# Kernel tuning notes

Measured on AMD Instinct MI355X. Metric: run time of the kernel, lower is better.

## Reference

```python
import jax, jax.numpy as jnp
import numpy as np

N, C, H, O, NUM_CLASSES = 4096, 768, 512, 50, 1


def setup_inputs() -> dict:
    key = jax.random.key(0)
    ks = jax.random.split(key, 8)
    x = jax.random.normal(ks[0], (N, C), dtype=jnp.float32)
    labels = jax.random.randint(ks[1], (N,), 0, 2, dtype=jnp.int64)
    W1 = jax.random.normal(ks[2], (C, H), dtype=jnp.float32) / np.sqrt(C)
    b1 = jnp.zeros((H,), dtype=jnp.float32)
    W2 = jax.random.normal(ks[3], (H, O), dtype=jnp.float32) / np.sqrt(H)
    b2 = jnp.zeros((O,), dtype=jnp.float32)
    fcW = jax.random.normal(ks[4], (C + O, NUM_CLASSES), dtype=jnp.float32) / np.sqrt(C + O)
    fcb = jnp.zeros((NUM_CLASSES,), dtype=jnp.float32)
    return {"x": x, "labels": labels, "W1": W1, "b1": b1, "W2": W2, "b2": b2, "fcW": fcW, "fcb": fcb}


def _build_graph(x, labels):
    # similarity-threshold edge construction (dense masked form of the python double loop)
    sim = x @ x.T                                   # [N, N]
    n = x.shape[0]
    diff = labels[:, None] != labels[None, :]       # cross-label pairs
    cnt = jnp.sum(diff)
    s = jnp.sum(jnp.where(diff, sim, 0.0))
    threshold = jnp.where(cnt > 0, s / cnt.astype(sim.dtype), jnp.asarray(0.0, sim.dtype))
    eye = jnp.eye(n, dtype=bool)
    same = (labels[:, None] == labels[None, :]) & ~eye
    edge_mask = same & (sim <= threshold)           # symmetric (sim symmetric)
    loss_mask = edge_mask & (jnp.arange(n)[:, None] < jnp.arange(n)[None, :])  # i<j pairs
    adj = jax.lax.stop_gradient(edge_mask.astype(x.dtype))
    # GCN normalization with self-loops
    a = adj + jnp.eye(n, dtype=x.dtype)
    dinv = jax.lax.rsqrt(jnp.sum(a, axis=1))        # deg >= 1
    norm_adj = dinv[:, None] * a * dinv[None, :]
    return norm_adj, loss_mask


def reference(x, labels, W1, b1, W2, b2, fcW, fcb):
    norm_adj, loss_mask = _build_graph(x, labels)
    h = jax.nn.relu(norm_adj @ (x @ W1) + b1)       # conv1 + relu
    g = norm_adj @ (h @ W2) + b2                    # conv2
    f_g = jnp.concatenate([x, g], axis=-1)          # [N, C+O]
    out = f_g @ fcW + fcb                           # [N, 1]
    return out, f_g, loss_mask, x
```

## Files before the change

kernel.cpp:

```cpp
#include <hip/hip_runtime.h>
#include <hip/hip_bf16.h>
#include <math.h>

#define NN 4096
#define CD 768
#define HD 512
#define OD 50
#define FGD 818

typedef short short8 __attribute__((ext_vector_type(8)));
typedef float f32x4 __attribute__((ext_vector_type(4)));
typedef unsigned short us4 __attribute__((ext_vector_type(4)));
typedef unsigned short ushortT;
typedef unsigned char uchar;
typedef unsigned long long u64;

__device__ inline ushortT f2bf(float v) {
    __hip_bfloat16 b = __float2bfloat16(v);
    return *(ushortT*)&b;
}
__device__ inline float bf2f(ushortT u) {
    __hip_bfloat16 b = *(__hip_bfloat16*)&u;
    return __bfloat162float(b);
}
__device__ inline float dinv_of(int d) {
    return (float)(1.0 / sqrt((double)(1 + d)));
}

__global__ __launch_bounds__(256) void gsum_kernel(const float* __restrict__ x,
                                                   const int* __restrict__ labels,
                                                   double* __restrict__ gsum) {
    int b = blockIdx.x;
    int t = threadIdx.x;
    double a0[3] = {0, 0, 0}, a1[3] = {0, 0, 0};
    for (int rr = 0; rr < 16; ++rr) {
        int row = b * 16 + rr;
        int lab = labels[row];
#pragma unroll
        for (int s = 0; s < 3; ++s) {
            double v = (double)x[(size_t)row * CD + t + s * 256];
            if (lab == 0) a0[s] += v; else a1[s] += v;
        }
    }
#pragma unroll
    for (int s = 0; s < 3; ++s) {
        atomicAdd(&gsum[t + s * 256], a0[s]);
        atomicAdd(&gsum[768 + t + s * 256], a1[s]);
    }
}

__global__ __launch_bounds__(256) void gdot_kernel(const double* __restrict__ gsum,
                                                   const int* __restrict__ labels,
                                                   double* __restrict__ scal) {
    int t = threadIdx.x;
    double d = 0.0;
    for (int c = t; c < CD; c += 256) d += gsum[c] * gsum[768 + c];
    int n0 = 0;
    for (int i = t; i < NN; i += 256) n0 += (labels[i] == 0) ? 1 : 0;
    for (int off = 32; off; off >>= 1) {
        d += __shfl_down(d, off);
        n0 += __shfl_down(n0, off);
    }
    __shared__ double sd[4];
    __shared__ int sn[4];
    int wid = t >> 6, lane = t & 63;
    if (lane == 0) { sd[wid] = d; sn[wid] = n0; }
    __syncthreads();
    if (t == 0) {
        double D = sd[0] + sd[1] + sd[2] + sd[3];
        double N0 = (double)(sn[0] + sn[1] + sn[2] + sn[3]);
        scal[0] = 2.0 * D;
        scal[1] = 2.0 * N0 * ((double)NN - N0);
    }
}

#define BAND 4e-3
#define RC_CAP (1 << 18)

__global__ __launch_bounds__(256) void sim_fused(
    const ushortT* __restrict__ xh, const ushortT* __restrict__ xl,
    const int* __restrict__ labels, const double* __restrict__ scal,
    u64* __restrict__ abbits, float* __restrict__ lm, int* __restrict__ deg,
    int* __restrict__ rc_cnt, int* __restrict__ rc_list) {
    int bid = blockIdx.x;
    int sid = (bid & 7) * 260 + (bid >> 3);
    int sby = 0, rem = sid;
    for (; sby < 8; ++sby) {
        int rowsz = 36 + (7 - sby) * 64;
        if (rem < rowsz) break;
        rem -= rowsz;
    }
    int sbx, iby, ibx;
    if (rem < 36) {
        sbx = sby;
        iby = 0;
        while (rem >= 8 - iby) { rem -= 8 - iby; ++iby; }
        ibx = iby + rem;
    } else {
        rem -= 36;
        sbx = sby + 1 + (rem >> 6);
        int u = rem & 63;
        iby = u >> 3; ibx = u & 7;
    }
    int by = sby * 8 + iby, bx = sbx * 8 + ibx;
    bool diag = (bx == by);

    __shared__ ushortT lds[4 * 64 * 72];
    __shared__ int larr[128];
    int tid = threadIdx.x;
    int lane = tid & 63;
    int w = tid >> 6;
    int wr = w >> 1, wc = w & 1;
    int m = lane & 15, quad = lane >> 4;
    int row0 = by * 64, col0 = bx * 64;

    if (tid < 64) larr[tid] = labels[row0 + tid];
    else if (tid < 128) larr[tid] = labels[col0 + tid - 64];

    f32x4 acc[2][2] = {{{0.f, 0.f, 0.f, 0.f}, {0.f, 0.f, 0.f, 0.f}},
                       {{0.f, 0.f, 0.f, 0.f}, {0.f, 0.f, 0.f, 0.f}}};

    const size_t rowbase = (size_t)row0 * CD;
    const size_t colbase = (size_t)col0 * CD;
    short8 rg[2][4];
#pragma unroll
    for (int tt = 0; tt < 2; ++tt) {
        int id2 = tid + tt * 256;
        int row = id2 >> 3, c8 = (id2 & 7) * 8;
        rg[tt][0] = *(const short8*)&xh[rowbase + (size_t)row * CD + c8];
        rg[tt][1] = *(const short8*)&xl[rowbase + (size_t)row * CD + c8];
        rg[tt][2] = *(const short8*)&xh[colbase + (size_t)row * CD + c8];
        rg[tt][3] = *(const short8*)&xl[colbase + (size_t)row * CD + c8];
    }

    for (int k0 = 0; k0 < CD; k0 += 64) {
        __syncthreads();
#pragma unroll
        for (int tt = 0; tt < 2; ++tt) {
            int id2 = tid + tt * 256;
            int row = id2 >> 3, c8 = (id2 & 7) * 8;
            *(short8*)&lds[0 * 4608 + row * 72 + c8] = rg[tt][0];
            *(short8*)&lds[1 * 4608 + row * 72 + c8] = rg[tt][1];
            *(short8*)&lds[2 * 4608 + row * 72 + c8] = rg[tt][2];
            *(short8*)&lds[3 * 4608 + row * 72 + c8] = rg[tt][3];
        }
        __syncthreads();
        if (k0 + 64 < CD) {
#pragma unroll
            for (int tt = 0; tt < 2; ++tt) {
                int id2 = tid + tt * 256;
                int row = id2 >> 3, c8 = (id2 & 7) * 8 + k0 + 64;
                rg[tt][0] = *(const short8*)&xh[rowbase + (size_t)row * CD + c8];
                rg[tt][1] = *(const short8*)&xl[rowbase + (size_t)row * CD + c8];
                rg[tt][2] = *(const short8*)&xh[colbase + (size_t)row * CD + c8];
                rg[tt][3] = *(const short8*)&xl[colbase + (size_t)row * CD + c8];
            }
        }
#pragma unroll
        for (int ks = 0; ks < 2; ++ks) {
            short8 ah[2], al[2], bh[2], bl[2];
#pragma unroll
            for (int i = 0; i < 2; ++i) {
                int ro = (wr * 32 + i * 16 + m) * 72 + ks * 32 + quad * 8;
                ah[i] = *(const short8*)&lds[0 * 4608 + ro];
                al[i] = *(const short8*)&lds[1 * 4608 + ro];
            }
#pragma unroll
            for (int j = 0; j < 2; ++j) {
                int co = (wc * 32 + j * 16 + m) * 72 + ks * 32 + quad * 8;
                bh[j] = *(const short8*)&lds[2 * 4608 + co];
                bl[j] = *(const short8*)&lds[3 * 4608 + co];
            }
#pragma unroll
            for (int i = 0; i < 2; ++i)
#pragma unroll
                for (int j = 0; j < 2; ++j) {
                    acc[i][j] = __builtin_amdgcn_mfma_f32_16x16x32_bf16(
                        ah[i], bh[j], acc[i][j], 0, 0, 0);
                    acc[i][j] = __builtin_amdgcn_mfma_f32_16x16x32_bf16(
                        ah[i], bl[j], acc[i][j], 0, 0, 0);
                    acc[i][j] = __builtin_amdgcn_mfma_f32_16x16x32_bf16(
                        al[i], bh[j], acc[i][j], 0, 0, 0);
                }
        }
    }
    __syncthreads();

    double thrd;
    {
        double cnt = scal[1];
        thrd = (cnt > 0.0) ? (scal[0] / cnt) : 0.0;
    }
    uchar* flags = (uchar*)lds;
#pragma unroll
    for (int i = 0; i < 2; ++i)
#pragma unroll
        for (int j = 0; j < 2; ++j) {
#pragma unroll
            for (int r = 0; r < 4; ++r) {
                int row = wr * 32 + i * 16 + quad * 4 + r;
                int col = wc * 32 + j * 16 + m;
                bool same = (larr[row] == larr[64 + col]);
                bool selfp = ((row0 + row) == (col0 + col));
                bool edge = false;
                if (same && !selfp) {
                    double s = (double)acc[i][j][r];
                    if (s <= thrd - BAND) {
                        edge = true;
                    } else if (s <= thrd + BAND) {
                        edge = (s <= thrd);
                        int enc = ((row0 + row) << 12) | (col0 + col) |
                                  (diag ? 0 : (1 << 24)) |
                                  (edge ? (1 << 25) : 0);
                        int idx = atomicAdd(rc_cnt, 1);
                        if (idx < RC_CAP) rc_list[idx] = enc;
                    }
                }
                flags[row * 68 + col] = edge ? 1 : 0;
            }
        }
    __syncthreads();

    {
        int r = tid >> 2, q = tid & 3;
        int cnti = 0;
        unsigned int bits16 = 0;
#pragma unroll
        for (int s = 0; s < 4; ++s) {
            int cb = q * 16 + s * 4;
            float4 f;
#pragma unroll
            for (int k2 = 0; k2 < 4; ++k2) {
                int c = cb + k2;
                bool fl = flags[r * 68 + c] != 0;
                cnti += fl ? 1 : 0;
                if (fl || (diag && r == c)) bits16 |= 1u << (s * 4 + k2);
                ((float*)&f)[k2] = (fl && (row0 + r < col0 + c)) ? 1.0f : 0.0f;
            }
            *(float4*)&lm[(size_t)(row0 + r) * NN + col0 + cb] = f;
        }
        unsigned int s1 = __shfl_down(bits16, 1);
        unsigned int s2 = __shfl_down(bits16, 2);
        unsigned int s3 = __shfl_down(bits16, 3);
        cnti += __shfl_down(cnti, 1);
        cnti += __shfl_down(cnti, 2);
        if (q == 0) {
            u64 u = (u64)bits16 | ((u64)s1 << 16) | ((u64)s2 << 32) |
                    ((u64)s3 << 48);
            abbits[(size_t)(row0 + r) * 64 + bx] = u;
            if (cnti) atomicAdd(&deg[row0 + r], cnti);
        }
    }

    if (!diag) {
        int c = tid >> 2, q = tid & 3;
        int cnti = 0;
        unsigned int bits16 = 0;
        float4 fz = {0.0f, 0.0f, 0.0f, 0.0f};
#pragma unroll
        for (int s = 0; s < 4; ++s) {
            int rb = q * 16 + s * 4;
#pragma unroll
            for (int k2 = 0; k2 < 4; ++k2) {
                bool fl = flags[(rb + k2) * 68 + c] != 0;
                cnti += fl ? 1 : 0;
                if (fl) bits16 |= 1u << (s * 4 + k2);
            }
            *(float4*)&lm[(size_t)(col0 + c) * NN + row0 + rb] = fz;
        }
        unsigned int s1 = __shfl_down(bits16, 1);
        unsigned int s2 = __shfl_down(bits16, 2);
        unsigned int s3 = __shfl_down(bits16, 3);
        cnti += __shfl_down(cnti, 1);
        cnti += __shfl_down(cnti, 2);
        if (q == 0) {
            u64 u = (u64)bits16 | ((u64)s1 << 16) | ((u64)s2 << 32) |
                    ((u64)s3 << 48);
            abbits[(size_t)(col0 + c) * 64 + by] = u;
            if (cnti) atomicAdd(&deg[col0 + c], cnti);
        }
    }
}

__global__ __launch_bounds__(256) void rc_fix(
    const float* __restrict__ x, const double* __restrict__ scal,
    const int* __restrict__ rc_cnt, const int* __restrict__ rc_list,
    u64* __restrict__ abbits, float* __restrict__ lm, int* __restrict__ deg) {
    int cnt = *rc_cnt;
    if (cnt > RC_CAP) cnt = RC_CAP;
    double thrd;
    {
        double c = scal[1];
        thrd = (c > 0.0) ? (scal[0] / c) : 0.0;
    }
    int lane = threadIdx.x & 63;
    int wid = (blockIdx.x * 256 + threadIdx.x) >> 6;
    int nw = (gridDim.x * 256) >> 6;
    for (int e = wid; e < cnt; e += nw) {
        int enc = rc_list[e];
        int c = enc & 0xFFF;
        int r = (enc >> 12) & 0xFFF;
        bool mirror = (enc >> 24) & 1;
        bool prov = (enc >> 25) & 1;
        const float* xi = x + (size_t)r * CD;
        const float* xj = x + (size_t)c * CD;
        double d = 0.0;
#pragma unroll
        for (int s = 0; s < 12; ++s)
            d += (double)xi[lane + s * 64] * (double)xj[lane + s * 64];
        for (int off = 32; off; off >>= 1) d += __shfl_down(d, off);
        if (lane == 0) {
            bool exact = (d <= thrd);
            if (exact != prov) {
                u64 mk = 1ull << (c & 63);
                if (exact) atomicOr(&abbits[(size_t)r * 64 + (c >> 6)], mk);
                else       atomicAnd(&abbits[(size_t)r * 64 + (c >> 6)], ~mk);
                lm[(size_t)r * NN + c] = (exact && r < c) ? 1.0f : 0.0f;
                int dlt = exact ? 1 : -1;
                atomicAdd(&deg[r], dlt);
                if (mirror) {
                    u64 mk2 = 1ull << (r & 63);
                    if (exact) atomicOr(&abbits[(size_t)c * 64 + (r >> 6)], mk2);
                    else       atomicAnd(&abbits[(size_t)c * 64 + (r >> 6)], ~mk2);
                    atomicAdd(&deg[c], dlt);
                }
            }
        }
    }
}

__global__ __launch_bounds__(256) void prep_kernel(
    const float* __restrict__ x, const float* __restrict__ W1,
    const float* __restrict__ W2, float* __restrict__ fg, float* __restrict__ xo,
    ushortT* __restrict__ xh, ushortT* __restrict__ xl, ushortT* __restrict__ w1t,
    ushortT* __restrict__ w2t) {
    int b = blockIdx.x;
    if (b < 4096) {
        int t = threadIdx.x;
        if (t < 192) {
            float4 v = *(const float4*)&x[(size_t)b * CD + t * 4];
            *(float4*)&xo[(size_t)b * CD + t * 4] = v;
            fg[(size_t)b * FGD + t * 4 + 0] = v.x;
            fg[(size_t)b * FGD + t * 4 + 1] = v.y;
            fg[(size_t)b * FGD + t * 4 + 2] = v.z;
            fg[(size_t)b * FGD + t * 4 + 3] = v.w;
            us4 hh, ll;
            float* vp = (float*)&v;
#pragma unroll
            for (int k = 0; k < 4; ++k) {
                ushortT h = f2bf(vp[k]);
                ((ushortT*)&hh)[k] = h;
                ((ushortT*)&ll)[k] = f2bf(vp[k] - bf2f(h));
            }
            *(us4*)&xh[(size_t)b * CD + t * 4] = hh;
            *(us4*)&xl[(size_t)b * CD + t * 4] = ll;
        }
        return;
    }
    __shared__ float tT[32][33];
    const float* P;
    ushortT* T;
    int K, N, Npad, k0, n0;
    if (b < 4480) {
        int bb = b - 4096;
        P = W1; T = w1t; K = CD; N = HD; Npad = HD;
        k0 = (bb % 24) * 32; n0 = (bb / 24) * 32;
    } else {
        int bb = b - 4480;
        P = W2; T = w2t; K = HD; N = OD; Npad = 64;
        k0 = (bb % 16) * 32; n0 = (bb / 16) * 32;
    }
    int tx = threadIdx.x & 31, ty = threadIdx.x >> 5;
#pragma unroll
    for (int s = 0; s < 4; ++s) {
        int k = k0 + ty + s * 8, n = n0 + tx;
        tT[ty + s * 8][tx] = (k < K && n < N) ? P[(size_t)k * N + n] : 0.0f;
    }
    __syncthreads();
#pragma unroll
    for (int s = 0; s < 4; ++s) {
        int n = n0 + ty + s * 8, k = k0 + tx;
        if (n < Npad && k < K) T[(size_t)n * K + k] = f2bf(tT[tx][ty + s * 8]);
    }
}

template <bool RELU, bool HASBIAS, int EPI>
__global__ __launch_bounds__(256) void gemm_bf16(
    const ushortT* __restrict__ A, const ushortT* __restrict__ B,
    ushortT* __restrict__ Cb, int M, int Nn, int K, int ldc,
    const int* __restrict__ deg, const float* __restrict__ bias) {
    __shared__ ushortT lds[2 * 64 * 72];
    int tid = threadIdx.x;
    int lane = tid & 63;
    int w = tid >> 6;
    int wr = w >> 1, wc = w & 1;
    int m = lane & 15, quad = lane >> 4;
    int row0 = blockIdx.y * 64, col0 = blockIdx.x * 64;

    f32x4 acc[2][2] = {{{0.f, 0.f, 0.f, 0.f}, {0.f, 0.f, 0.f, 0.f}},
                       {{0.f, 0.f, 0.f, 0.f}, {0.f, 0.f, 0.f, 0.f}}};

    for (int k0 = 0; k0 < K; k0 += 64) {
#pragma unroll
        for (int t = 0; t < 2; ++t) {
            int id2 = tid + t * 256;
            int row = id2 >> 3, c8 = (id2 & 7) * 8;
            *(short8*)&lds[row * 72 + c8] =
                *(const short8*)&A[(size_t)(row0 + row) * K + k0 + c8];
            *(short8*)&lds[4608 + row * 72 + c8] =
                *(const short8*)&B[(size_t)(col0 + row) * K + k0 + c8];
        }
        __syncthreads();
#pragma unroll
        for (int ks = 0; ks < 2; ++ks) {
            short8 af[2], bf[2];
#pragma unroll
            for (int i = 0; i < 2; ++i)
                af[i] = *(const short8*)&lds[(wr * 32 + i * 16 + m) * 72 +
                                             ks * 32 + quad * 8];
#pragma unroll
            for (int j = 0; j < 2; ++j)
                bf[j] = *(const short8*)&lds[4608 + (wc * 32 + j * 16 + m) * 72 +
                                             ks * 32 + quad * 8];
#pragma unroll
            for (int i = 0; i < 2; ++i)
#pragma unroll
                for (int j = 0; j < 2; ++j)
                    acc[i][j] = __builtin_amdgcn_mfma_f32_16x16x32_bf16(
                        af[i], bf[j], acc[i][j], 0, 0, 0);
        }
        __syncthreads();
    }

    if (EPI == 2) {
        ushortT* Th = lds;
#pragma unroll
        for (int i = 0; i < 2; ++i)
#pragma unroll
            for (int j = 0; j < 2; ++j)
#pragma unroll
                for (int r = 0; r < 4; ++r) {
                    int row = wr * 32 + i * 16 + quad * 4 + r;
                    int col = wc * 32 + j * 16 + m;
                    float dv = dinv_of(deg[row0 + row]);
                    Th[col * 72 + row] = f2bf(acc[i][j][r] * dv);
                }
        __syncthreads();
#pragma unroll
        for (int t = 0; t < 2; ++t) {
            int id2 = tid + t * 256;
            int cc = id2 >> 3, chunk = id2 & 7;
            *(short8*)&Cb[(size_t)(col0 + cc) * M + row0 + chunk * 8] =
                *(const short8*)&Th[cc * 72 + chunk * 8];
        }
    } else {
#pragma unroll
        for (int i = 0; i < 2; ++i)
#pragma unroll
            for (int j = 0; j < 2; ++j)
#pragma unroll
                for (int r = 0; r < 4; ++r) {
                    int row = wr * 32 + i * 16 + quad * 4 + r;
                    int col = wc * 32 + j * 16 + m;
                    int gr = row0 + row, gc = col0 + col;
                    if (gc < Nn) {
                        float v = acc[i][j][r] * dinv_of(deg[gr]);
                        if (HASBIAS) v += bias[gc];
                        if (RELU) v = fmaxf(v, 0.0f);
                        Cb[(size_t)gr * ldc + gc] = f2bf(v);
                    }
                }
    }
}

__global__ __launch_bounds__(256) void gemm_part(
    const ushortT* __restrict__ A, const ushortT* __restrict__ B,
    float* __restrict__ P, int M, int K, int KC) {
    __shared__ ushortT lds[2 * 64 * 72];
    int tid = threadIdx.x;
    int lane = tid & 63;
    int w = tid >> 6;
    int wr = w >> 1, wc = w & 1;
    int m = lane & 15, quad = lane >> 4;
    int kb = blockIdx.x;
    int row0 = blockIdx.y * 64;
    int kbase = kb * KC;

    f32x4 acc[2][2] = {{{0.f, 0.f, 0.f, 0.f}, {0.f, 0.f, 0.f, 0.f}},
                       {{0.f, 0.f, 0.f, 0.f}, {0.f, 0.f, 0.f, 0.f}}};

    for (int k0 = 0; k0 < KC; k0 += 64) {
#pragma unroll
        for (int t = 0; t < 2; ++t) {
            int id2 = tid + t * 256;
            int row = id2 >> 3, c8 = (id2 & 7) * 8;
            *(short8*)&lds[row * 72 + c8] =
                *(const short8*)&A[(size_t)(row0 + row) * K + kbase + k0 + c8];
            *(short8*)&lds[4608 + row * 72 + c8] =
                *(const short8*)&B[(size_t)row * K + kbase + k0 + c8];
        }
        __syncthreads();
#pragma unroll
        for (int ks = 0; ks < 2; ++ks) {
            short8 af[2], bf[2];
#pragma unroll
            for (int i = 0; i < 2; ++i)
                af[i] = *(const short8*)&lds[(wr * 32 + i * 16 + m) * 72 +
                                             ks * 32 + quad * 8];
#pragma unroll
            for (int j = 0; j < 2; ++j)
                bf[j] = *(const short8*)&lds[4608 + (wc * 32 + j * 16 + m) * 72 +
                                             ks * 32 + quad * 8];
#pragma unroll
            for (int i = 0; i < 2; ++i)
#pragma unroll
                for (int j = 0; j < 2; ++j)
                    acc[i][j] = __builtin_amdgcn_mfma_f32_16x16x32_bf16(
                        af[i], bf[j], acc[i][j], 0, 0, 0);
        }
        __syncthreads();
    }
#pragma unroll
    for (int i = 0; i < 2; ++i)
#pragma unroll
        for (int j = 0; j < 2; ++j)
#pragma unroll
            for (int r = 0; r < 4; ++r) {
                int row = wr * 32 + i * 16 + quad * 4 + r;
                int col = wc * 32 + j * 16 + m;
                P[((size_t)kb * M + row0 + row) * 64 + col] = acc[i][j][r];
            }
}

__global__ __launch_bounds__(256) void gemm_partB(
    const u64* __restrict__ Abits, const ushortT* __restrict__ B,
    float* __restrict__ P, int M, int K, int KC) {
    __shared__ ushortT lds[2 * 64 * 72];
    int tid = threadIdx.x;
    int lane = tid & 63;
    int w = tid >> 6;
    int wr = w >> 1, wc = w & 1;
    int m = lane & 15, quad = lane >> 4;
    int kb = blockIdx.x;
    int row0 = blockIdx.y * 64;
    int kbase = kb * KC;
    int er = tid >> 2, eq = tid & 3;

    f32x4 acc[2][2] = {{{0.f, 0.f, 0.f, 0.f}, {0.f, 0.f, 0.f, 0.f}},
                       {{0.f, 0.f, 0.f, 0.f}, {0.f, 0.f, 0.f, 0.f}}};

    for (int k0 = 0; k0 < KC; k0 += 64) {
#pragma unroll
        for (int t = 0; t < 2; ++t) {
            int id2 = tid + t * 256;
            int row = id2 >> 3, c8 = (id2 & 7) * 8;
            *(short8*)&lds[4608 + row * 72 + c8] =
                *(const short8*)&B[(size_t)row * K + kbase + k0 + c8];
        }
        {
            u64 bits = Abits[(size_t)(row0 + er) * 64 + ((kbase + k0) >> 6)];
            unsigned int half = (unsigned int)(bits >> (eq * 16)) & 0xFFFFu;
            short8 v0, v1;
#pragma unroll
            for (int k = 0; k < 8; ++k) {
                ((ushortT*)&v0)[k] =
                    ((half >> k) & 1) ? (ushortT)0x3F80 : (ushortT)0;
                ((ushortT*)&v1)[k] =
                    ((half >> (k + 8)) & 1) ? (ushortT)0x3F80 : (ushortT)0;
            }
            *(short8*)&lds[er * 72 + eq * 16] = v0;
            *(short8*)&lds[er * 72 + eq * 16 + 8] = v1;
        }
        __syncthreads();
#pragma unroll
        for (int ks = 0; ks < 2; ++ks) {
            short8 af[2], bf[2];
#pragma unroll
            for (int i = 0; i < 2; ++i)
                af[i] = *(const short8*)&lds[(wr * 32 + i * 16 + m) * 72 +
                                             ks * 32 + quad * 8];
#pragma unroll
            for (int j = 0; j < 2; ++j)
                bf[j] = *(const short8*)&lds[4608 + (wc * 32 + j * 16 + m) * 72 +
                                             ks * 32 + quad * 8];
#pragma unroll
            for (int i = 0; i < 2; ++i)
#pragma unroll
                for (int j = 0; j < 2; ++j)
                    acc[i][j] = __builtin_amdgcn_mfma_f32_16x16x32_bf16(
                        af[i], bf[j], acc[i][j], 0, 0, 0);
        }
        __syncthreads();
    }
#pragma unroll
    for (int i = 0; i < 2; ++i)
#pragma unroll
        for (int j = 0; j < 2; ++j)
#pragma unroll
            for (int r = 0; r < 4; ++r) {
                int row = wr * 32 + i * 16 + quad * 4 + r;
                int col = wc * 32 + j * 16 + m;
                P[((size_t)kb * M + row0 + row) * 64 + col] = acc[i][j][r];
            }
}

__global__ __launch_bounds__(256) void gemm_partWB(
    const u64* __restrict__ Abits, const ushortT* __restrict__ B,
    float* __restrict__ P, int M, int K, int KC, int ldP) {
    __shared__ ushortT lds[2 * 64 * 72];
    int tid = threadIdx.x;
    int lane = tid & 63;
    int w = tid >> 6;
    int wr = w >> 1, wc = w & 1;
    int m = lane & 15, quad = lane >> 4;
    int col0 = blockIdx.x * 64;
    int row0 = blockIdx.y * 64;
    int kb = blockIdx.z;
    int kbase = kb * KC;
    int er = tid >> 2, eq = tid & 3;

    f32x4 acc[2][2] = {{{0.f, 0.f, 0.f, 0.f}, {0.f, 0.f, 0.f, 0.f}},
                       {{0.f, 0.f, 0.f, 0.f}, {0.f, 0.f, 0.f, 0.f}}};

    for (int k0 = 0; k0 < KC; k0 += 64) {
#pragma unroll
        for (int t = 0; t < 2; ++t) {
            int id2 = tid + t * 256;
            int row = id2 >> 3, c8 = (id2 & 7) * 8;
            *(short8*)&lds[4608 + row * 72 + c8] =
                *(const short8*)&B[(size_t)(col0 + row) * K + kbase + k0 + c8];
        }
        {
            u64 bits = Abits[(size_t)(row0 + er) * 64 + ((kbase + k0) >> 6)];
            unsigned int half = (unsigned int)(bits >> (eq * 16)) & 0xFFFFu;
            short8 v0, v1;
#pragma unroll
            for (int k = 0; k < 8; ++k) {
                ((ushortT*)&v0)[k] =
                    ((half >> k) & 1) ? (ushortT)0x3F80 : (ushortT)0;
                ((ushortT*)&v1)[k] =
                    ((half >> (k + 8)) & 1) ? (ushortT)0x3F80 : (ushortT)0;
            }
            *(short8*)&lds[er * 72 + eq * 16] = v0;
            *(short8*)&lds[er * 72 + eq * 16 + 8] = v1;
        }
        __syncthreads();
#pragma unroll
        for (int ks = 0; ks < 2; ++ks) {
            short8 af[2], bf[2];
#pragma unroll
            for (int i = 0; i < 2; ++i)
                af[i] = *(const short8*)&lds[(wr * 32 + i * 16 + m) * 72 +
                                             ks * 32 + quad * 8];
#pragma unroll
            for (int j = 0; j < 2; ++j)
                bf[j] = *(const short8*)&lds[4608 + (wc * 32 + j * 16 + m) * 72 +
                                             ks * 32 + quad * 8];
#pragma unroll
            for (int i = 0; i < 2; ++i)
#pragma unroll
                for (int j = 0; j < 2; ++j)
                    acc[i][j] = __builtin_amdgcn_mfma_f32_16x16x32_bf16(
                        af[i], bf[j], acc[i][j], 0, 0, 0);
        }
        __syncthreads();
    }
#pragma unroll
    for (int i = 0; i < 2; ++i)
#pragma unroll
        for (int j = 0; j < 2; ++j)
#pragma unroll
            for (int r = 0; r < 4; ++r) {
                int row = wr * 32 + i * 16 + quad * 4 + r;
                int col = wc * 32 + j * 16 + m;
                P[((size_t)kb * M + row0 + row) * ldP + col0 + col] =
                    acc[i][j][r];
            }
}

__global__ __launch_bounds__(256) void k5_epi(const float* __restrict__ P5,
                                              const int* __restrict__ deg,
                                              const float* __restrict__ b1,
                                              ushortT* __restrict__ hb) {
    int tid = threadIdx.x;
    int cg = tid & 127;
    int rr = tid >> 7;
#pragma unroll
    for (int p = 0; p < 2; ++p) {
        int r = blockIdx.x * 4 + p * 2 + rr;
        float dv = dinv_of(deg[r]);
        float4 s = {0.f, 0.f, 0.f, 0.f};
#pragma unroll
        for (int kb = 0; kb < 4; ++kb) {
            float4 v = *(const float4*)&P5[((size_t)kb * NN + r) * HD + cg * 4];
            s.x += v.x; s.y += v.y; s.z += v.z; s.w += v.w;
        }
        float4 bv = *(const float4*)&b1[cg * 4];
        us4 o;
        o[0] = f2bf(fmaxf(s.x * dv + bv.x, 0.f));
        o[1] = f2bf(fmaxf(s.y * dv + bv.y, 0.f));
        o[2] = f2bf(fmaxf(s.z * dv + bv.z, 0.f));
        o[3] = f2bf(fmaxf(s.w * dv + bv.w, 0.f));
        *(us4*)&hb[(size_t)r * HD + cg * 4] = o;
    }
}

__global__ __launch_bounds__(256) void k6_epi(const float* __restrict__ P6,
                                              const int* __restrict__ deg,
                                              ushortT* __restrict__ hw2sT) {
    __shared__ ushortT Th[64 * 72];
    int row0 = blockIdx.x * 64;
    int tid = threadIdx.x;
    int rl = tid >> 2, q = tid & 3;
    float dv = dinv_of(deg[row0 + rl]);
#pragma unroll
    for (int s = 0; s < 16; ++s) {
        int c = q * 16 + s;
        float v = 0.f;
#pragma unroll
        for (int kb = 0; kb < 4; ++kb)
            v += P6[((size_t)kb * NN + row0 + rl) * 64 + c];
        Th[c * 72 + rl] = f2bf(v * dv);
    }
    __syncthreads();
#pragma unroll
    for (int t = 0; t < 2; ++t) {
        int id2 = tid + t * 256;
        int cc = id2 >> 3, chunk = id2 & 7;
        *(short8*)&hw2sT[(size_t)cc * NN + row0 + chunk * 8] =
            *(const short8*)&Th[cc * 72 + chunk * 8];
    }
}

__global__ __launch_bounds__(256) void k7_epi_out(
    const float* __restrict__ P7, const int* __restrict__ deg,
    const float* __restrict__ b2, const float* __restrict__ fcW,
    const float* __restrict__ fcb, float* __restrict__ fg,
    float* __restrict__ out) {
    int row0 = blockIdx.x * 64;
    int tid = threadIdx.x;
    int rl = tid >> 2, q = tid & 3;
    int r = row0 + rl;
    float dv = dinv_of(deg[r]);
    float sg = 0.f;
#pragma unroll
    for (int s = 0; s < 16; ++s) {
        int c = q * 16 + s;
        if (c < OD) {
            float v = 0.f;
#pragma unroll
            for (int kb = 0; kb < 8; ++kb)
                v += P7[((size_t)kb * NN + r) * 64 + c];
            v = v * dv + b2[c];
            fg[(size_t)r * FGD + CD + c] = v;
            sg += v * fcW[CD + c];
        }
    }
    const float* fr = fg + (size_t)r * FGD;
    float sx = 0.f;
    for (int k = q * 192; k < (q + 1) * 192; k += 2) {
        float2 vv = *(const float2*)&fr[k];
        float2 ww = *(const float2*)&fcW[k];
        sx += vv.x * ww.x + vv.y * ww.y;
    }
    float s = sx + sg;
    s += __shfl_down(s, 1);
    s += __shfl_down(s, 2);
    if (q == 0) out[r] = s + fcb[0];
}

extern "C" void kernel_launch(void* const* d_in, const int* in_sizes, int n_in,
                              void* d_out, int out_size, void* d_ws, size_t ws_size,
                              hipStream_t stream) {
    const float* x = (const float*)d_in[0];
    const int* labels = (const int*)d_in[1];
    const float* W1 = (const float*)d_in[2];
    const float* b1 = (const float*)d_in[3];
    const float* W2 = (const float*)d_in[4];
    const float* b2 = (const float*)d_in[5];
    const float* fcW = (const float*)d_in[6];
    const float* fcb = (const float*)d_in[7];
    float* outp = (float*)d_out;

    const size_t o_out = 0;
    const size_t o_fg = 4096;
    const size_t o_lm = o_fg + (size_t)NN * FGD;
    const size_t o_x = o_lm + (size_t)NN * NN;

    char* ws = (char*)d_ws;
    size_t off = 0;
    u64* abbits = (u64*)(ws + off); off += (size_t)NN * 64 * 8;
    ushortT* xh = (ushortT*)(ws + off); off += (size_t)NN * CD * 2;
    ushortT* xl = (ushortT*)(ws + off); off += (size_t)NN * CD * 2;
    ushortT* w1t = (ushortT*)(ws + off); off += (size_t)HD * CD * 2;
    ushortT* xw1sT = (ushortT*)(ws + off); off += (size_t)HD * NN * 2;
    ushortT* hb = (ushortT*)(ws + off); off += (size_t)NN * HD * 2;
    ushortT* w2t = (ushortT*)(ws + off); off += (size_t)64 * HD * 2;
    ushortT* hw2sT = (ushortT*)(ws + off); off += (size_t)64 * NN * 2;
    char* zbase = ws + off;
    int* deg = (int*)(ws + off); off += (size_t)NN * 4;
    double* gsum = (double*)(ws + off); off += 1536 * 8;
    double* scal = (double*)(ws + off); off += 16;
    int* rc_cnt = (int*)(ws + off); off += 16;
    size_t zbytes = (size_t)NN * 4 + 1536 * 8 + 16 + 16;
    char* uni = ws + off;
    int* rc_list = (int*)uni;
    float* P5 = (float*)uni;
    float* P6 = (float*)uni;
    float* P7 = (float*)uni;
    off += (size_t)4 * NN * HD * 4;

    hipMemsetAsync(zbase, 0, zbytes, stream);

    prep_kernel<<<4512, 256, 0, stream>>>(x, W1, W2, outp + o_fg, outp + o_x, xh, xl,
                                          w1t, w2t);

    gsum_kernel<<<256, 256, 0, stream>>>(x, labels, gsum);
    gdot_kernel<<<1, 256, 0, stream>>>(gsum, labels, scal);

    sim_fused<<<2080, 256, 0, stream>>>(xh, xl, labels, scal, abbits, outp + o_lm,
                                        deg, rc_cnt, rc_list);

    rc_fix<<<512, 256, 0, stream>>>(x, scal, rc_cnt, rc_list, abbits, outp + o_lm,
                                    deg);

    gemm_bf16<false, false, 2><<<dim3(HD / 64, NN / 64), 256, 0, stream>>>(
        xh, w1t, xw1sT, NN, HD, CD, 0, deg, nullptr);

    gemm_partWB<<<dim3(HD / 64, NN / 64, 4), 256, 0, stream>>>(
        abbits, xw1sT, P5, NN, NN, NN / 4, HD);
    k5_epi<<<NN / 4, 256, 0, stream>>>(P5, deg, b1, hb);

    gemm_part<<<dim3(4, NN / 64), 256, 0, stream>>>(hb, w2t, P6, NN, HD, HD / 4);
    k6_epi<<<NN / 64, 256, 0, stream>>>(P6, deg, hw2sT);

    gemm_partB<<<dim3(8, NN / 64), 256, 0, stream>>>(abbits, hw2sT, P7, NN, NN,
                                                     NN / 8);
    k7_epi_out<<<NN / 64, 256, 0, stream>>>(P7, deg, b2, fcW, fcb, outp + o_fg,
                                            outp + o_out);
}
```

Baseline: 322.2 us.

## Use single fp16 MFMA for similarity GEMM and widen split-K partitions

Replaces the three-pass bf16 hi/lo split product in the similarity kernel with one fp16 MFMA pass on an fp16 copy of x. This cuts MFMA work, LDS footprint and global loads by roughly half or more. The recheck band widens from 4e-3 to 0.10 so the rc_fix pass can correct borderline threshold decisions, which may push far more pairs into that exact-recheck path. Separately, split-K factors for the conv2 GEMMs double (4→8 and 8→16 partitions) to add parallelism, with the epilogues summing more partials.

Result: slower. 424.8 us (+31.8%).

```diff
diff --git a/kernel.cpp b/kernel.cpp
--- a/kernel.cpp
+++ b/kernel.cpp
@@ -9,6 +9,7 @@
 #define FGD 818
 
 typedef short short8 __attribute__((ext_vector_type(8)));
+typedef _Float16 half8 __attribute__((ext_vector_type(8)));
 typedef float f32x4 __attribute__((ext_vector_type(4)));
 typedef unsigned short us4 __attribute__((ext_vector_type(4)));
 typedef unsigned short ushortT;
@@ -74,13 +75,13 @@
     }
 }
 
-#define BAND 4e-3
+#define BAND 0.10
 #define RC_CAP (1 << 18)
 
 __global__ __launch_bounds__(256) void sim_fused(
-    const ushortT* __restrict__ xh, const ushortT* __restrict__ xl,
-    const int* __restrict__ labels, const double* __restrict__ scal,
-    u64* __restrict__ abbits, float* __restrict__ lm, int* __restrict__ deg,
+    const ushortT* __restrict__ xf, const int* __restrict__ labels,
+    const double* __restrict__ scal, u64* __restrict__ abbits,
+    float* __restrict__ lm, int* __restrict__ deg,
     int* __restrict__ rc_cnt, int* __restrict__ rc_list) {
     int bid = blockIdx.x;
     int sid = (bid & 7) * 260 + (bid >> 3);
@@ -105,7 +106,7 @@
     int by = sby * 8 + iby, bx = sbx * 8 + ibx;
     bool diag = (bx == by);
 
-    __shared__ ushortT lds[4 * 64 * 72];
+    __shared__ ushortT lds[2 * 64 * 72];
     __shared__ int larr[128];
     int tid = threadIdx.x;
     int lane = tid & 63;
@@ -122,15 +123,13 @@
 
     const size_t rowbase = (size_t)row0 * CD;
     const size_t colbase = (size_t)col0 * CD;
-    short8 rg[2][4];
+    short8 rg[2][2];
 #pragma unroll
     for (int tt = 0; tt < 2; ++tt) {
         int id2 = tid + tt * 256;
         int row = id2 >> 3, c8 = (id2 & 7) * 8;
-        rg[tt][0] = *(const short8*)&xh[rowbase + (size_t)row * CD + c8];
-        rg[tt][1] = *(const short8*)&xl[rowbase + (size_t)row * CD + c8];
-        rg[tt][2] = *(const short8*)&xh[colbase + (size_t)row * CD + c8];
-        rg[tt][3] = *(const short8*)&xl[colbase + (size_t)row * CD + c8];
+        rg[tt][0] = *(const short8*)&xf[rowbase + (size_t)row * CD + c8];
+        rg[tt][1] = *(const short8*)&xf[colbase + (size_t)row * CD + c8];
     }
 
     for (int k0 = 0; k0 < CD; k0 += 64) {
@@ -141,8 +140,6 @@
             int row = id2 >> 3, c8 = (id2 & 7) * 8;
             *(short8*)&lds[0 * 4608 + row * 72 + c8] = rg[tt][0];
             *(short8*)&lds[1 * 4608 + row * 72 + c8] = rg[tt][1];
-            *(short8*)&lds[2 * 4608 + row * 72 + c8] = rg[tt][2];
-            *(short8*)&lds[3 * 4608 + row * 72 + c8] = rg[tt][3];
         }
         __syncthreads();
         if (k0 + 64 < CD) {
@@ -150,38 +147,27 @@
             for (int tt = 0; tt < 2; ++tt) {
                 int id2 = tid + tt * 256;
                 int row = id2 >> 3, c8 = (id2 & 7) * 8 + k0 + 64;
-                rg[tt][0] = *(const short8*)&xh[rowbase + (size_t)row * CD + c8];
-                rg[tt][1] = *(const short8*)&xl[rowbase + (size_t)row * CD + c8];
-                rg[tt][2] = *(const short8*)&xh[colbase + (size_t)row * CD + c8];
-                rg[tt][3] = *(const short8*)&xl[colbase + (size_t)row * CD + c8];
+                rg[tt][0] = *(const short8*)&xf[rowbase + (size_t)row * CD + c8];
+                rg[tt][1] = *(const short8*)&xf[colbase + (size_t)row * CD + c8];
             }
         }
 #pragma unroll
         for (int ks = 0; ks < 2; ++ks) {
-            short8 ah[2], al[2], bh[2], bl[2];
-#pragma unroll
-            for (int i = 0; i < 2; ++i) {
-                int ro = (wr * 32 + i * 16 + m) * 72 + ks * 32 + quad * 8;
-                ah[i] = *(const short8*)&lds[0 * 4608 + ro];
-                al[i] = *(const short8*)&lds[1 * 4608 + ro];
-            }
-#pragma unroll
-            for (int j = 0; j < 2; ++j) {
-                int co = (wc * 32 + j * 16 + m) * 72 + ks * 32 + quad * 8;
-                bh[j] = *(const short8*)&lds[2 * 4608 + co];
-                bl[j] = *(const short8*)&lds[3 * 4608 + co];
-            }
-#pragma unroll
-            for (int i = 0; i < 2; ++i)
-#pragma unroll
-                for (int j = 0; j < 2; ++j) {
-                    acc[i][j] = __builtin_amdgcn_mfma_f32_16x16x32_bf16(
+            half8 ah[2], bh[2];
+#pragma unroll
+            for (int i = 0; i < 2; ++i)
+                ah[i] = *(const half8*)&lds[(wr * 32 + i * 16 + m) * 72 +
+                                            ks * 32 + quad * 8];
+#pragma unroll
+            for (int j = 0; j < 2; ++j)
+                bh[j] = *(const half8*)&lds[4608 + (wc * 32 + j * 16 + m) * 72 +
+                                            ks * 32 + quad * 8];
+#pragma unroll
+            for (int i = 0; i < 2; ++i)
+#pragma unroll
+                for (int j = 0; j < 2; ++j)
+                    acc[i][j] = __builtin_amdgcn_mfma_f32_16x16x32_f16(
                         ah[i], bh[j], acc[i][j], 0, 0, 0);
-                    acc[i][j] = __builtin_amdgcn_mfma_f32_16x16x32_bf16(
-                        ah[i], bl[j], acc[i][j], 0, 0, 0);
-                    acc[i][j] = __builtin_amdgcn_mfma_f32_16x16x32_bf16(
-                        al[i], bh[j], acc[i][j], 0, 0, 0);
-                }
         }
     }
     __syncthreads();
@@ -332,7 +318,7 @@
 __global__ __launch_bounds__(256) void prep_kernel(
     const float* __restrict__ x, const float* __restrict__ W1,
     const float* __restrict__ W2, float* __restrict__ fg, float* __restrict__ xo,
-    ushortT* __restrict__ xh, ushortT* __restrict__ xl, ushortT* __restrict__ w1t,
+    ushortT* __restrict__ xh, ushortT* __restrict__ xf, ushortT* __restrict__ w1t,
     ushortT* __restrict__ w2t) {
     int b = blockIdx.x;
     if (b < 4096) {
@@ -344,16 +330,16 @@
             fg[(size_t)b * FGD + t * 4 + 1] = v.y;
             fg[(size_t)b * FGD + t * 4 + 2] = v.z;
             fg[(size_t)b * FGD + t * 4 + 3] = v.w;
-            us4 hh, ll;
+            us4 hh, ff;
             float* vp = (float*)&v;
 #pragma unroll
             for (int k = 0; k < 4; ++k) {
-                ushortT h = f2bf(vp[k]);
-                ((ushortT*)&hh)[k] = h;
-                ((ushortT*)&ll)[k] = f2bf(vp[k] - bf2f(h));
+                ((ushortT*)&hh)[k] = f2bf(vp[k]);
+                _Float16 g = (_Float16)vp[k];
+                ((ushortT*)&ff)[k] = *(ushortT*)&g;
             }
             *(us4*)&xh[(size_t)b * CD + t * 4] = hh;
-            *(us4*)&xl[(size_t)b * CD + t * 4] = ll;
+            *(us4*)&xf[(size_t)b * CD + t * 4] = ff;
         }
         return;
     }
@@ -718,7 +704,7 @@
         int c = q * 16 + s;
         float v = 0.f;
 #pragma unroll
-        for (int kb = 0; kb < 4; ++kb)
+        for (int kb = 0; kb < 8; ++kb)
             v += P6[((size_t)kb * NN + row0 + rl) * 64 + c];
         Th[c * 72 + rl] = f2bf(v * dv);
     }
@@ -749,7 +735,7 @@
         if (c < OD) {
             float v = 0.f;
 #pragma unroll
-            for (int kb = 0; kb < 8; ++kb)
+            for (int kb = 0; kb < 16; ++kb)
                 v += P7[((size_t)kb * NN + r) * 64 + c];
             v = v * dv + b2[c];
             fg[(size_t)r * FGD + CD + c] = v;
@@ -791,7 +777,7 @@
     size_t off = 0;
     u64* abbits = (u64*)(ws + off); off += (size_t)NN * 64 * 8;
     ushortT* xh = (ushortT*)(ws + off); off += (size_t)NN * CD * 2;
-    ushortT* xl = (ushortT*)(ws + off); off += (size_t)NN * CD * 2;
+    ushortT* xf = (ushortT*)(ws + off); off += (size_t)NN * CD * 2;
     ushortT* w1t = (ushortT*)(ws + off); off += (size_t)HD * CD * 2;
     ushortT* xw1sT = (ushortT*)(ws + off); off += (size_t)HD * NN * 2;
     ushortT* hb = (ushortT*)(ws + off); off += (size_t)NN * HD * 2;
@@ -812,13 +798,13 @@
 
     hipMemsetAsync(zbase, 0, zbytes, stream);
 
-    prep_kernel<<<4512, 256, 0, stream>>>(x, W1, W2, outp + o_fg, outp + o_x, xh, xl,
+    prep_kernel<<<4512, 256, 0, stream>>>(x, W1, W2, outp + o_fg, outp + o_x, xh, xf,
                                           w1t, w2t);
 
     gsum_kernel<<<256, 256, 0, stream>>>(x, labels, gsum);
     gdot_kernel<<<1, 256, 0, stream>>>(gsum, labels, scal);
 
-    sim_fused<<<2080, 256, 0, stream>>>(xh, xl, labels, scal, abbits, outp + o_lm,
+    sim_fused<<<2080, 256, 0, stream>>>(xf, labels, scal, abbits, outp + o_lm,
                                         deg, rc_cnt, rc_list);
 
     rc_fix<<<512, 256, 0, stream>>>(x, scal, rc_cnt, rc_list, abbits, outp + o_lm,
@@ -831,11 +817,11 @@
         abbits, xw1sT, P5, NN, NN, NN / 4, HD);
     k5_epi<<<NN / 4, 256, 0, stream>>>(P5, deg, b1, hb);
 
-    gemm_part<<<dim3(4, NN / 64), 256, 0, stream>>>(hb, w2t, P6, NN, HD, HD / 4);
+    gemm_part<<<dim3(8, NN / 64), 256, 0, stream>>>(hb, w2t, P6, NN, HD, HD / 8);
     k6_epi<<<NN / 64, 256, 0, stream>>>(P6, deg, hw2sT);
 
-    gemm_partB<<<dim3(8, NN / 64), 256, 0, stream>>>(abbits, hw2sT, P7, NN, NN,
-                                                     NN / 8);
+    gemm_partB<<<dim3(16, NN / 64), 256, 0, stream>>>(abbits, hw2sT, P7, NN, NN,
+                                                      NN / 16);
     k7_epi_out<<<NN / 64, 256, 0, stream>>>(P7, deg, b2, fcW, fcb, outp + o_fg,
                                             outp + o_out);
 }
```
